# Performance work log

Hardware: AMD Instinct MI355X
Metric: run time of the kernel (lower is better)

## Reference

```python
import jax, jax.numpy as jnp
import numpy as np

D_MODEL = 2048
D_STATE = 16
KER = 4
DT_RANK = D_MODEL // 16  # mamba default: ceil(d_model/16) = 128
B_SZ = 2
SEQ = 1024


def setup_inputs() -> dict:
    key = jax.random.key(0)
    ks = jax.random.split(key, 8)
    s = 0.02
    return {
        "x": jax.random.normal(ks[0], (B_SZ, SEQ, D_MODEL), jnp.float32),
        # in_proj: d_model -> 2*d_inner (expand=1 so d_inner=d_model)
        "W_in": jax.random.normal(ks[1], (2 * D_MODEL, D_MODEL), jnp.float32) * s,
        # depthwise causal conv, one kernel of length KER per channel
        "conv_w": jax.random.normal(ks[2], (D_MODEL, KER), jnp.float32) * s,
        "conv_b": jnp.zeros((D_MODEL,), jnp.float32),
        # x_proj: d_inner -> dt_rank + 2*d_state
        "W_xproj": jax.random.normal(ks[3], (DT_RANK + 2 * D_STATE, D_MODEL), jnp.float32) * s,
        # dt_proj: dt_rank -> d_inner
        "W_dt": jax.random.normal(ks[4], (D_MODEL, DT_RANK), jnp.float32) * s,
        "b_dt": jax.random.uniform(ks[5], (D_MODEL,), jnp.float32, -4.0, -2.0),
        # S4D-real init: A = -[1..d_state] per channel, stored as log
        "A_log": jnp.log(jnp.broadcast_to(jnp.arange(1, D_STATE + 1, dtype=jnp.float32), (D_MODEL, D_STATE))),
        "Dskip": jnp.ones((D_MODEL,), jnp.float32),
        # out_proj: d_inner -> d_model
        "W_out": jax.random.normal(ks[6], (D_MODEL, D_MODEL), jnp.float32) * s,
    }


def _mamba(x, W_in, conv_w, conv_b, W_xproj, W_dt, b_dt, A_log, Dskip, W_out):
    Bsz, L, dm = x.shape
    d_state = A_log.shape[1]
    dt_rank = W_dt.shape[1]
    K = conv_w.shape[1]

    # in_proj -> gate z and ssm input u
    xz = x @ W_in.T                      # [B, L, 2*d_inner]
    u, z = jnp.split(xz, 2, axis=-1)     # each [B, L, d_inner]

    # causal depthwise conv1d over time, then SiLU
    up = jnp.pad(u, ((0, 0), (K - 1, 0), (0, 0)))
    conv = conv_b + sum(conv_w[:, k] * up[:, k:k + L, :] for k in range(K))
    u = jax.nn.silu(conv)                # [B, L, d_inner]

    # input-dependent dt, B, C
    x_dbl = u @ W_xproj.T                # [B, L, dt_rank + 2*d_state]
    dt_r = x_dbl[..., :dt_rank]
    Bm = x_dbl[..., dt_rank:dt_rank + d_state]      # [B, L, N]
    Cm = x_dbl[..., dt_rank + d_state:]             # [B, L, N]
    dt = jax.nn.softplus(dt_r @ W_dt.T + b_dt)      # [B, L, d_inner]

    A = -jnp.exp(A_log)                             # [d_inner, N]
    dA = jnp.exp(dt[..., None] * A)                 # [B, L, d_inner, N]
    dBu = dt[..., None] * Bm[:, :, None, :] * u[..., None]  # [B, L, d_inner, N]

    def step(h, inp):
        dA_t, dBu_t, C_t = inp
        h = dA_t * h + dBu_t                        # [B, d_inner, N]
        y_t = jnp.einsum('bdn,bn->bd', h, C_t)      # [B, d_inner]
        return h, y_t

    h0 = jnp.zeros((Bsz, dm, d_state), dtype=x.dtype)
    _, ys = jax.lax.scan(step, h0,
                         (dA.swapaxes(0, 1), dBu.swapaxes(0, 1), Cm.swapaxes(0, 1)))
    y = ys.swapaxes(0, 1) + u * Dskip               # [B, L, d_inner]
    y = y * jax.nn.silu(z)
    return y @ W_out.T                              # [B, L, d_model]


def reference(x, W_in, conv_w, conv_b, W_xproj, W_dt, b_dt, A_log, Dskip, W_out):
    return _mamba(x, W_in, conv_w, conv_b, W_xproj, W_dt, b_dt, A_log, Dskip, W_out)
```

## Files before the change

### kernel.cpp

```cpp
#include <hip/hip_runtime.h>
#include <hip/hip_bf16.h>


#define D_MODEL 2048
#define D_STATE 16
#define KER 4
#define DT_RANK 128
#define B_SZ 2
#define SEQ 1024
#define BL (B_SZ * SEQ)
#define XPROJ_N (DT_RANK + 2 * D_STATE)
#define NC 32
#define TC (SEQ / NC)

using f32x4  = __attribute__((ext_vector_type(4))) float;
using bf16x8 = __attribute__((ext_vector_type(8))) __bf16;
using bf16x4 = __attribute__((ext_vector_type(4))) __bf16;

__device__ __forceinline__ float softplusf(float x) {
    return (x > 20.f) ? x : log1pf(__expf(x));
}
__device__ __forceinline__ float siluf(float x) {
    return x / (1.f + __expf(-x));
}

__global__ __launch_bounds__(256) void split_kernel(
    const float* __restrict__ src,
    __bf16* __restrict__ hi, __bf16* __restrict__ lo, int n4)
{
    int i = blockIdx.x * 256 + threadIdx.x;
    if (i >= n4) return;
    float4 v = *reinterpret_cast<const float4*>(&src[(size_t)i * 4]);
    bf16x4 hv, lv;
    float f[4] = {v.x, v.y, v.z, v.w};
    #pragma unroll
    for (int j = 0; j < 4; ++j) {
        __bf16 h = (__bf16)f[j];
        hv[j] = h;
        lv[j] = (__bf16)(f[j] - (float)h);
    }
    *reinterpret_cast<bf16x4*>(&hi[(size_t)i * 4]) = hv;
    *reinterpret_cast<bf16x4*>(&lo[(size_t)i * 4]) = lv;
}

__global__ __launch_bounds__(256, 2) void gemm_bf3(
    const __bf16* __restrict__ Ah, const __bf16* __restrict__ Al,
    const __bf16* __restrict__ Wh, const __bf16* __restrict__ Wl,
    float* __restrict__ C, int N_, int K)
{
    __shared__ __align__(16) __bf16 lds[4 * 128 * 64];
    __bf16* sAh = lds;
    __bf16* sAl = lds + 8192;
    __bf16* sWh = lds + 16384;
    __bf16* sWl = lds + 24576;

    const int tid = threadIdx.x;
    const int bm = blockIdx.y * 128;
    const int bn = blockIdx.x * 128;
    const int w  = tid >> 6;
    const int l  = tid & 63;
    const int wr = (w >> 1) * 64;
    const int wc = (w & 1) * 64;
    const int fr = l & 15;
    const int fq = l >> 4;

    f32x4 acc[4][4] = {};

    for (int k0 = 0; k0 < K; k0 += 64) {
        #pragma unroll
        for (int i = 0; i < 4; ++i) {
            const int f  = i * 256 + tid;
            const int r  = f >> 3;
            const int ss = f & 7;
            const int gs = ss ^ (r & 7);
            const size_t ga = (size_t)(bm + r) * K + k0 + gs * 8;
            const size_t gw = (size_t)(bn + r) * K + k0 + gs * 8;
            __builtin_amdgcn_global_load_lds(
                (const __attribute__((address_space(1))) void*)(Ah + ga),
                (__attribute__((address_space(3))) void*)(sAh + (size_t)f * 8), 16, 0, 0);
            __builtin_amdgcn_global_load_lds(
                (const __attribute__((address_space(1))) void*)(Al + ga),
                (__attribute__((address_space(3))) void*)(sAl + (size_t)f * 8), 16, 0, 0);
            __builtin_amdgcn_global_load_lds(
                (const __attribute__((address_space(1))) void*)(Wh + gw),
                (__attribute__((address_space(3))) void*)(sWh + (size_t)f * 8), 16, 0, 0);
            __builtin_amdgcn_global_load_lds(
                (const __attribute__((address_space(1))) void*)(Wl + gw),
                (__attribute__((address_space(3))) void*)(sWl + (size_t)f * 8), 16, 0, 0);
        }
        __syncthreads();

        #pragma unroll
        for (int ks = 0; ks < 2; ++ks) {
            bf16x8 ah[4], al[4], wh[4], wl[4];
            #pragma unroll
            for (int t = 0; t < 4; ++t) {
                const int ra = wr + t * 16 + fr;
                const int sa = (ks * 4 + fq) ^ (ra & 7);
                ah[t] = *reinterpret_cast<const bf16x8*>(&sAh[ra * 64 + sa * 8]);
                al[t] = *reinterpret_cast<const bf16x8*>(&sAl[ra * 64 + sa * 8]);
                const int rw = wc + t * 16 + fr;
                const int sw = (ks * 4 + fq) ^ (rw & 7);
                wh[t] = *reinterpret_cast<const bf16x8*>(&sWh[rw * 64 + sw * 8]);
                wl[t] = *reinterpret_cast<const bf16x8*>(&sWl[rw * 64 + sw * 8]);
            }
            #pragma unroll
            for (int mt = 0; mt < 4; ++mt)
                #pragma unroll
                for (int nt = 0; nt < 4; ++nt) {
                    acc[mt][nt] = __builtin_amdgcn_mfma_f32_16x16x32_bf16(
                        ah[mt], wh[nt], acc[mt][nt], 0, 0, 0);
                    acc[mt][nt] = __builtin_amdgcn_mfma_f32_16x16x32_bf16(
                        ah[mt], wl[nt], acc[mt][nt], 0, 0, 0);
                    acc[mt][nt] = __builtin_amdgcn_mfma_f32_16x16x32_bf16(
                        al[mt], wh[nt], acc[mt][nt], 0, 0, 0);
                }
        }
        __syncthreads();
    }

    #pragma unroll
    for (int mt = 0; mt < 4; ++mt)
        #pragma unroll
        for (int nt = 0; nt < 4; ++nt)
            #pragma unroll
            for (int j = 0; j < 4; ++j)
                C[(size_t)(bm + wr + mt * 16 + fq * 4 + j) * N_
                  + bn + wc + nt * 16 + fr] = acc[mt][nt][j];
}

#define BM 64
#define BN 64
#define BKT 32

template <int EPI>
__global__ __launch_bounds__(256) void gemm_nt(
    const float* __restrict__ A, int lda,
    const float* __restrict__ W, int ldw,
    float* __restrict__ C, int ldc,
    const float* __restrict__ bias,
    int M, int N, int K)
{
    __shared__ float As[BKT][BM + 4];
    __shared__ float Ws[BKT][BN + 4];

    const int tid = threadIdx.x;
    const int bm = blockIdx.y * BM;
    const int bn = blockIdx.x * BN;
    const int tx = tid & 15;
    const int ty = tid >> 4;

    float acc[4][4] = {};

    for (int k0 = 0; k0 < K; k0 += BKT) {
        #pragma unroll
        for (int i = 0; i < 2; ++i) {
            int f = tid + i * 256;
            int row = f >> 3;
            int kq  = f & 7;
            float4 v = *reinterpret_cast<const float4*>(
                &A[(size_t)(bm + row) * lda + k0 + kq * 4]);
            As[kq * 4 + 0][row] = v.x;
            As[kq * 4 + 1][row] = v.y;
            As[kq * 4 + 2][row] = v.z;
            As[kq * 4 + 3][row] = v.w;
        }
        #pragma unroll
        for (int i = 0; i < 2; ++i) {
            int f = tid + i * 256;
            int row = f >> 3;
            int kq  = f & 7;
            int gn = bn + row;
            float4 v = make_float4(0.f, 0.f, 0.f, 0.f);
            if (gn < N) {
                v = *reinterpret_cast<const float4*>(
                    &W[(size_t)gn * ldw + k0 + kq * 4]);
            }
            Ws[kq * 4 + 0][row] = v.x;
            Ws[kq * 4 + 1][row] = v.y;
            Ws[kq * 4 + 2][row] = v.z;
            Ws[kq * 4 + 3][row] = v.w;
        }
        __syncthreads();

        #pragma unroll
        for (int kk = 0; kk < BKT; ++kk) {
            float4 a4 = *reinterpret_cast<const float4*>(&As[kk][ty * 4]);
            float4 w4 = *reinterpret_cast<const float4*>(&Ws[kk][tx * 4]);
            float a[4] = {a4.x, a4.y, a4.z, a4.w};
            float wv[4] = {w4.x, w4.y, w4.z, w4.w};
            #pragma unroll
            for (int i = 0; i < 4; ++i)
                #pragma unroll
                for (int j = 0; j < 4; ++j)
                    acc[i][j] = fmaf(a[i], wv[j], acc[i][j]);
        }
        __syncthreads();
    }

    #pragma unroll
    for (int i = 0; i < 4; ++i) {
        int gm = bm + ty * 4 + i;
        #pragma unroll
        for (int j = 0; j < 4; ++j) {
            int gn = bn + tx * 4 + j;
            if (gn < N) {
                float v = acc[i][j];
                if (EPI == 1) v = softplusf(v + bias[gn]);
                C[(size_t)gm * ldc + gn] = v;
            }
        }
    }
}

#define XBM 64
#define XBN 32
#define XKS 8
#define XKC (D_MODEL / XKS)

__global__ __launch_bounds__(256) void xdbl_partial(
    const float* __restrict__ A,
    const float* __restrict__ W,
    float* __restrict__ P)
{
    __shared__ float As[BKT][XBM + 4];
    __shared__ float Ws[BKT][XBN + 4];

    const int tid = threadIdx.x;
    const int bm = blockIdx.y * XBM;
    const int bn = blockIdx.x * XBN;
    const int ks = blockIdx.z;
    const int tx = tid & 7;
    const int ty = tid >> 3;

    float acc[2][4] = {};

    const int kend = (ks + 1) * XKC;
    for (int k0 = ks * XKC; k0 < kend; k0 += BKT) {
        #pragma unroll
        for (int i = 0; i < 2; ++i) {
            int f = tid + i * 256;
            int row = f >> 3;
            int kq  = f & 7;
            float4 v = *reinterpret_cast<const float4*>(
                &A[(size_t)(bm + row) * D_MODEL + k0 + kq * 4]);
            As[kq * 4 + 0][row] = v.x;
            As[kq * 4 + 1][row] = v.y;
            As[kq * 4 + 2][row] = v.z;
            As[kq * 4 + 3][row] = v.w;
        }
        {
            int row = tid >> 3;
            int kq  = tid & 7;
            float4 v = *reinterpret_cast<const float4*>(
                &W[(size_t)(bn + row) * D_MODEL + k0 + kq * 4]);
            Ws[kq * 4 + 0][row] = v.x;
            Ws[kq * 4 + 1][row] = v.y;
            Ws[kq * 4 + 2][row] = v.z;
            Ws[kq * 4 + 3][row] = v.w;
        }
        __syncthreads();

        #pragma unroll
        for (int kk = 0; kk < BKT; ++kk) {
            float a0 = As[kk][ty * 2 + 0];
            float a1 = As[kk][ty * 2 + 1];
            float4 w4 = *reinterpret_cast<const float4*>(&Ws[kk][tx * 4]);
            float wv[4] = {w4.x, w4.y, w4.z, w4.w};
            #pragma unroll
            for (int j = 0; j < 4; ++j) {
                acc[0][j] = fmaf(a0, wv[j], acc[0][j]);
                acc[1][j] = fmaf(a1, wv[j], acc[1][j]);
            }
        }
        __syncthreads();
    }

    #pragma unroll
    for (int i = 0; i < 2; ++i) {
        const int gm = bm + ty * 2 + i;
        #pragma unroll
        for (int j = 0; j < 4; ++j) {
            const int gn = bn + tx * 4 + j;
            P[((size_t)ks * BL + gm) * XPROJ_N + gn] = acc[i][j];
        }
    }
}

__global__ __launch_bounds__(256) void xdbl_reduce(
    const float* __restrict__ P, float* __restrict__ xdbl)
{
    const int i = blockIdx.x * 256 + threadIdx.x;
    const int n4 = BL * XPROJ_N / 4;
    if (i >= n4) return;
    float4 s = *reinterpret_cast<const float4*>(&P[(size_t)i * 4]);
    #pragma unroll
    for (int ks = 1; ks < XKS; ++ks) {
        float4 v = *reinterpret_cast<const float4*>(
            &P[(size_t)ks * BL * XPROJ_N + (size_t)i * 4]);
        s.x += v.x; s.y += v.y; s.z += v.z; s.w += v.w;
    }
    *reinterpret_cast<float4*>(&xdbl[(size_t)i * 4]) = s;
}

__global__ __launch_bounds__(256) void conv_silu_kernel(
    const float* __restrict__ xz,
    const float* __restrict__ conv_w,
    const float* __restrict__ conv_b,
    float* __restrict__ u)
{
    int idx = blockIdx.x * 256 + threadIdx.x;
    if (idx >= BL * (D_MODEL / 4)) return;
    const int d4 = (idx & (D_MODEL / 4 - 1)) * 4;
    const int bl = idx >> 9;
    const int l  = bl & (SEQ - 1);
    const int b  = bl >> 10;

    float4 cb = *reinterpret_cast<const float4*>(&conv_b[d4]);
    float4 cw[4];
    #pragma unroll
    for (int j = 0; j < 4; ++j)
        cw[j] = *reinterpret_cast<const float4*>(&conv_w[(d4 + j) * KER]);

    float acc[4] = {cb.x, cb.y, cb.z, cb.w};
    #pragma unroll
    for (int k = 0; k < KER; ++k) {
        const int ls = l - (KER - 1) + k;
        if (ls >= 0) {
            float4 v = *reinterpret_cast<const float4*>(
                &xz[(size_t)(b * SEQ + ls) * (2 * D_MODEL) + d4]);
            acc[0] = fmaf((&cw[0].x)[k], v.x, acc[0]);
            acc[1] = fmaf((&cw[1].x)[k], v.y, acc[1]);
            acc[2] = fmaf((&cw[2].x)[k], v.z, acc[2]);
            acc[3] = fmaf((&cw[3].x)[k], v.w, acc[3]);
        }
    }
    float4 o;
    o.x = siluf(acc[0]); o.y = siluf(acc[1]);
    o.z = siluf(acc[2]); o.w = siluf(acc[3]);
    *reinterpret_cast<float4*>(&u[(size_t)bl * D_MODEL + d4]) = o;
}

__global__ __launch_bounds__(256) void scan_part1(
    const float* __restrict__ dt,
    const float* __restrict__ xdbl,
    const float* __restrict__ u,
    const float* __restrict__ A_log,
    float* __restrict__ PH,
    float* __restrict__ Hend)
{
    const int tid = threadIdx.x;
    const int d   = blockIdx.x * 256 + tid;
    const int bc  = blockIdx.y;
    const int b   = bc >> 5;
    const int c   = bc & (NC - 1);

    float A[16];
    #pragma unroll
    for (int q = 0; q < 4; ++q) {
        float4 v = *reinterpret_cast<const float4*>(&A_log[d * 16 + q * 4]);
        A[q*4+0] = -__expf(v.x); A[q*4+1] = -__expf(v.y);
        A[q*4+2] = -__expf(v.z); A[q*4+3] = -__expf(v.w);
    }
    float h[16] = {};
    float P[16];
    #pragma unroll
    for (int n = 0; n < 16; ++n) P[n] = 1.f;

    const size_t row0 = (size_t)b * SEQ + c * TC;
    for (int t = 0; t < TC; ++t) {
        const size_t row = row0 + t;
        const float dtv = dt[row * D_MODEL + d];
        const float uv  = u[row * D_MODEL + d];
        float Bv[16];
        const float4* Bp = reinterpret_cast<const float4*>(&xdbl[row * XPROJ_N + DT_RANK]);
        #pragma unroll
        for (int q = 0; q < 4; ++q) {
            float4 v = Bp[q];
            Bv[q*4+0] = v.x; Bv[q*4+1] = v.y; Bv[q*4+2] = v.z; Bv[q*4+3] = v.w;
        }
        const float dtu = dtv * uv;
        #pragma unroll
        for (int n = 0; n < 16; ++n) {
            float dA = __expf(dtv * A[n]);
            h[n] = fmaf(dA, h[n], dtu * Bv[n]);
            P[n] *= dA;
        }
    }
    const size_t off = ((size_t)bc * D_MODEL + d) * 16;
    #pragma unroll
    for (int q = 0; q < 4; ++q) {
        *reinterpret_cast<float4*>(&PH[off + q*4])   =
            make_float4(P[q*4+0], P[q*4+1], P[q*4+2], P[q*4+3]);
        *reinterpret_cast<float4*>(&Hend[off + q*4]) =
            make_float4(h[q*4+0], h[q*4+1], h[q*4+2], h[q*4+3]);
    }
}

__global__ __launch_bounds__(256) void scan_part2(
    float* __restrict__ PH,
    const float* __restrict__ Hend)
{
    const int g  = blockIdx.x * 256 + threadIdx.x;
    const int b  = g >> 15;
    const int dn = g & 32767;
    float h = 0.f;
    #pragma unroll
    for (int c = 0; c < NC; ++c) {
        const size_t off = ((size_t)(b * NC + c) * D_MODEL * 16) + dn;
        const float p  = PH[off];
        const float he = Hend[off];
        PH[off] = h;
        h = fmaf(p, h, he);
    }
}

__global__ __launch_bounds__(256) void scan_part3(
    const float* __restrict__ dt,
    const float* __restrict__ xdbl,
    const float* __restrict__ xz,
    const float* __restrict__ u,
    const float* __restrict__ A_log,
    const float* __restrict__ Dskip,
    const float* __restrict__ PH,
    __bf16* __restrict__ yh, __bf16* __restrict__ yl)
{
    const int tid = threadIdx.x;
    const int d   = blockIdx.x * 256 + tid;
    const int bc  = blockIdx.y;
    const int b   = bc >> 5;
    const int c   = bc & (NC - 1);

    float A[16];
    #pragma unroll
    for (int q = 0; q < 4; ++q) {
        float4 v = *reinterpret_cast<const float4*>(&A_log[d * 16 + q * 4]);
        A[q*4+0] = -__expf(v.x); A[q*4+1] = -__expf(v.y);
        A[q*4+2] = -__expf(v.z); A[q*4+3] = -__expf(v.w);
    }
    float h[16];
    const size_t off = ((size_t)bc * D_MODEL + d) * 16;
    #pragma unroll
    for (int q = 0; q < 4; ++q) {
        float4 v = *reinterpret_cast<const float4*>(&PH[off + q*4]);
        h[q*4+0] = v.x; h[q*4+1] = v.y; h[q*4+2] = v.z; h[q*4+3] = v.w;
    }
    const float Dk = Dskip[d];

    const size_t row0 = (size_t)b * SEQ + c * TC;
    for (int t = 0; t < TC; ++t) {
        const size_t row = row0 + t;
        const float dtv = dt[row * D_MODEL + d];
        const float uv  = u[row * D_MODEL + d];
        float Bv[16], Cv[16];
        const float4* Bp = reinterpret_cast<const float4*>(&xdbl[row * XPROJ_N + DT_RANK]);
        const float4* Cp = reinterpret_cast<const float4*>(&xdbl[row * XPROJ_N + DT_RANK + D_STATE]);
        #pragma unroll
        for (int q = 0; q < 4; ++q) {
            float4 v = Bp[q];
            Bv[q*4+0] = v.x; Bv[q*4+1] = v.y; Bv[q*4+2] = v.z; Bv[q*4+3] = v.w;
            float4 wv = Cp[q];
            Cv[q*4+0] = wv.x; Cv[q*4+1] = wv.y; Cv[q*4+2] = wv.z; Cv[q*4+3] = wv.w;
        }
        const float dtu = dtv * uv;
        float y = 0.f;
        #pragma unroll
        for (int n = 0; n < 16; ++n) {
            float dA = __expf(dtv * A[n]);
            h[n] = fmaf(dA, h[n], dtu * Bv[n]);
            y = fmaf(h[n], Cv[n], y);
        }
        const float zv = xz[row * (2 * D_MODEL) + D_MODEL + d];
        const float yv = (y + uv * Dk) * siluf(zv);
        const __bf16 hv = (__bf16)yv;
        yh[row * D_MODEL + d] = hv;
        yl[row * D_MODEL + d] = (__bf16)(yv - (float)hv);
    }
}

extern "C" void kernel_launch(void* const* d_in, const int* in_sizes, int n_in,
                              void* d_out, int out_size, void* d_ws, size_t ws_size,
                              hipStream_t stream) {
    const float* x       = (const float*)d_in[0];
    const float* W_in    = (const float*)d_in[1];
    const float* conv_w  = (const float*)d_in[2];
    const float* conv_b  = (const float*)d_in[3];
    const float* W_xproj = (const float*)d_in[4];
    const float* W_dt    = (const float*)d_in[5];
    const float* b_dt    = (const float*)d_in[6];
    const float* A_log   = (const float*)d_in[7];
    const float* Dskip   = (const float*)d_in[8];
    const float* W_out   = (const float*)d_in[9];
    float* out = (float*)d_out;

    float* ws = (float*)d_ws;
    const size_t M1 = 1024 * 1024;
    float* xz   = ws;
    float* u    = ws + 8 * M1;
    float* xdbl = ws + 12 * M1;
    float* dt   = ws + 12 * M1 + 512 * 1024;
    float* PH   = dt + 4 * M1;
    float* Hend = PH + 2 * M1;

    __bf16* planes = (__bf16*)(ws + 25 * M1);
    __bf16* xh  = planes;
    __bf16* xl  = xh + 4 * M1;
    __bf16* wih = xl + 4 * M1;
    __bf16* wil = wih + 8 * M1;
    __bf16* woh = wih;
    __bf16* wol = wih + 4 * M1;
    __bf16* yh  = xh;
    __bf16* yl  = xl;
    float* xpart = (float*)(ws + 25 * M1);

    split_kernel<<<(BL * D_MODEL / 4 + 255) / 256, 256, 0, stream>>>(x, xh, xl, BL * D_MODEL / 4);
    split_kernel<<<(2 * D_MODEL * D_MODEL / 4 + 255) / 256, 256, 0, stream>>>(
        W_in, wih, wil, 2 * D_MODEL * D_MODEL / 4);

    {
        dim3 grid(2 * D_MODEL / 128, BL / 128);
        gemm_bf3<<<grid, 256, 0, stream>>>(xh, xl, wih, wil, xz, 2 * D_MODEL, D_MODEL);
    }
    conv_silu_kernel<<<BL * (D_MODEL / 4) / 256, 256, 0, stream>>>(xz, conv_w, conv_b, u);

    split_kernel<<<(D_MODEL * D_MODEL / 4 + 255) / 256, 256, 0, stream>>>(
        W_out, woh, wol, D_MODEL * D_MODEL / 4);

    {
        dim3 grid(XPROJ_N / XBN, BL / XBM, XKS);
        xdbl_partial<<<grid, 256, 0, stream>>>(u, W_xproj, xpart);
        xdbl_reduce<<<(BL * XPROJ_N / 4 + 255) / 256, 256, 0, stream>>>(xpart, xdbl);
    }
    {
        dim3 grid(D_MODEL / BN, BL / BM);
        gemm_nt<1><<<grid, 256, 0, stream>>>(xdbl, XPROJ_N, W_dt, DT_RANK,
                                             dt, D_MODEL, b_dt,
                                             BL, D_MODEL, DT_RANK);
    }
    {
        dim3 grid(D_MODEL / 256, B_SZ * NC);
        scan_part1<<<grid, 256, 0, stream>>>(dt, xdbl, u, A_log, PH, Hend);
        scan_part2<<<B_SZ * D_MODEL * 16 / 256, 256, 0, stream>>>(PH, Hend);
        scan_part3<<<grid, 256, 0, stream>>>(dt, xdbl, xz, u, A_log, Dskip, PH, yh, yl);
    }
    {
        dim3 grid(D_MODEL / 128, BL / 128);
        gemm_bf3<<<grid, 256, 0, stream>>>(yh, yl, woh, wol, out, D_MODEL, D_MODEL);
    }
}
```

Measured before the change: 403.5 us.

## Use 32x32x16 MFMA in split-bf16 GEMM, remap workgroups, fuse split kernels

The 3-pass split-bf16 GEMM moves from 16x16x32 to 32x32x16 MFMA tiles (2x2 per wave), which changes the LDS fragment loads and the output write mapping. It also adds an XCD-aware remap of workgroup IDs so neighbouring tiles share L2, and merges the x and W_in bf16 split kernels into one grid-stride launch. The aim is fewer LDS reads per MFMA, better cache locality across chiplets and one less launch. The risks are register pressure from 16-wide accumulators and the remap formula assuming the tile count divides evenly by 8.

```diff
diff --git a/kernel.cpp b/kernel.cpp
--- a/kernel.cpp
+++ b/kernel.cpp
@@ -14,6 +14,7 @@
 #define TC (SEQ / NC)
 
 using f32x4  = __attribute__((ext_vector_type(4))) float;
+using f32x16 = __attribute__((ext_vector_type(16))) float;
 using bf16x8 = __attribute__((ext_vector_type(8))) __bf16;
 using bf16x4 = __attribute__((ext_vector_type(4))) __bf16;
 
@@ -24,12 +25,9 @@
     return x / (1.f + __expf(-x));
 }
 
-__global__ __launch_bounds__(256) void split_kernel(
-    const float* __restrict__ src,
-    __bf16* __restrict__ hi, __bf16* __restrict__ lo, int n4)
-{
-    int i = blockIdx.x * 256 + threadIdx.x;
-    if (i >= n4) return;
+__device__ __forceinline__ void split4(const float* __restrict__ src,
+                                       __bf16* __restrict__ hi,
+                                       __bf16* __restrict__ lo, int i) {
     float4 v = *reinterpret_cast<const float4*>(&src[(size_t)i * 4]);
     bf16x4 hv, lv;
     float f[4] = {v.x, v.y, v.z, v.w};
@@ -41,6 +39,28 @@
     }
     *reinterpret_cast<bf16x4*>(&hi[(size_t)i * 4]) = hv;
     *reinterpret_cast<bf16x4*>(&lo[(size_t)i * 4]) = lv;
+}
+
+__global__ __launch_bounds__(256) void split_kernel(
+    const float* __restrict__ src,
+    __bf16* __restrict__ hi, __bf16* __restrict__ lo, int n4)
+{
+    int i = blockIdx.x * 256 + threadIdx.x;
+    if (i >= n4) return;
+    split4(src, hi, lo, i);
+}
+
+__global__ __launch_bounds__(256) void split_xwi_kernel(
+    const float* __restrict__ x,  __bf16* __restrict__ xh,  __bf16* __restrict__ xl,
+    const float* __restrict__ wi, __bf16* __restrict__ wih, __bf16* __restrict__ wil)
+{
+    const int NX = BL * D_MODEL / 4;
+    const int NI = 2 * D_MODEL * D_MODEL / 4;
+    const int total = NX + NI;
+    for (int i = blockIdx.x * 256 + threadIdx.x; i < total; i += gridDim.x * 256) {
+        if (i < NX) split4(x, xh, xl, i);
+        else        split4(wi, wih, wil, i - NX);
+    }
 }
 
 __global__ __launch_bounds__(256, 2) void gemm_bf3(
@@ -55,16 +75,21 @@
     __bf16* sWl = lds + 24576;
 
     const int tid = threadIdx.x;
-    const int bm = blockIdx.y * 128;
-    const int bn = blockIdx.x * 128;
+
+    const int nwg = gridDim.x * gridDim.y;
+    const int fid = blockIdx.y * gridDim.x + blockIdx.x;
+    const int nid = (fid & 7) * (nwg >> 3) + (fid >> 3);
+    const int bm = (nid / gridDim.x) * 128;
+    const int bn = (nid % gridDim.x) * 128;
+
     const int w  = tid >> 6;
     const int l  = tid & 63;
     const int wr = (w >> 1) * 64;
     const int wc = (w & 1) * 64;
-    const int fr = l & 15;
-    const int fq = l >> 4;
-
-    f32x4 acc[4][4] = {};
+    const int lr = l & 31;
+    const int kg = l >> 5;
+
+    f32x16 acc[2][2] = {};
 
     for (int k0 = 0; k0 < K; k0 += 64) {
         #pragma unroll
@@ -91,28 +116,29 @@
         __syncthreads();
 
         #pragma unroll
-        for (int ks = 0; ks < 2; ++ks) {
-            bf16x8 ah[4], al[4], wh[4], wl[4];
+        for (int ks = 0; ks < 4; ++ks) {
+            const int slot = ks * 2 + kg;
+            bf16x8 ah[2], al[2], wh[2], wl[2];
             #pragma unroll
-            for (int t = 0; t < 4; ++t) {
-                const int ra = wr + t * 16 + fr;
-                const int sa = (ks * 4 + fq) ^ (ra & 7);
+            for (int t = 0; t < 2; ++t) {
+                const int ra = wr + t * 32 + lr;
+                const int sa = slot ^ (ra & 7);
                 ah[t] = *reinterpret_cast<const bf16x8*>(&sAh[ra * 64 + sa * 8]);
                 al[t] = *reinterpret_cast<const bf16x8*>(&sAl[ra * 64 + sa * 8]);
-                const int rw = wc + t * 16 + fr;
-                const int sw = (ks * 4 + fq) ^ (rw & 7);
+                const int rw = wc + t * 32 + lr;
+                const int sw = slot ^ (rw & 7);
                 wh[t] = *reinterpret_cast<const bf16x8*>(&sWh[rw * 64 + sw * 8]);
                 wl[t] = *reinterpret_cast<const bf16x8*>(&sWl[rw * 64 + sw * 8]);
             }
             #pragma unroll
-            for (int mt = 0; mt < 4; ++mt)
+            for (int mt = 0; mt < 2; ++mt)
                 #pragma unroll
-                for (int nt = 0; nt < 4; ++nt) {
-                    acc[mt][nt] = __builtin_amdgcn_mfma_f32_16x16x32_bf16(
+                for (int nt = 0; nt < 2; ++nt) {
+                    acc[mt][nt] = __builtin_amdgcn_mfma_f32_32x32x16_bf16(
                         ah[mt], wh[nt], acc[mt][nt], 0, 0, 0);
-                    acc[mt][nt] = __builtin_amdgcn_mfma_f32_16x16x32_bf16(
+                    acc[mt][nt] = __builtin_amdgcn_mfma_f32_32x32x16_bf16(
                         ah[mt], wl[nt], acc[mt][nt], 0, 0, 0);
-                    acc[mt][nt] = __builtin_amdgcn_mfma_f32_16x16x32_bf16(
+                    acc[mt][nt] = __builtin_amdgcn_mfma_f32_32x32x16_bf16(
                         al[mt], wh[nt], acc[mt][nt], 0, 0, 0);
                 }
         }
@@ -120,13 +146,15 @@
     }
 
     #pragma unroll
-    for (int mt = 0; mt < 4; ++mt)
-        #pragma unroll
-        for (int nt = 0; nt < 4; ++nt)
+    for (int mt = 0; mt < 2; ++mt)
+        #pragma unroll
+        for (int nt = 0; nt < 2; ++nt)
             #pragma unroll
-            for (int j = 0; j < 4; ++j)
-                C[(size_t)(bm + wr + mt * 16 + fq * 4 + j) * N_
-                  + bn + wc + nt * 16 + fr] = acc[mt][nt][j];
+            for (int reg = 0; reg < 16; ++reg) {
+                const int row = (reg & 3) + 8 * (reg >> 2) + 4 * kg;
+                C[(size_t)(bm + wr + mt * 32 + row) * N_
+                  + bn + wc + nt * 32 + lr] = acc[mt][nt][reg];
+            }
 }
 
 #define BM 64
@@ -513,9 +541,7 @@
     __bf16* yl  = xl;
     float* xpart = (float*)(ws + 25 * M1);
 
-    split_kernel<<<(BL * D_MODEL / 4 + 255) / 256, 256, 0, stream>>>(x, xh, xl, BL * D_MODEL / 4);
-    split_kernel<<<(2 * D_MODEL * D_MODEL / 4 + 255) / 256, 256, 0, stream>>>(
-        W_in, wih, wil, 2 * D_MODEL * D_MODEL / 4);
+    split_xwi_kernel<<<2048, 256, 0, stream>>>(x, xh, xl, W_in, wih, wil);
 
     {
         dim3 grid(2 * D_MODEL / 128, BL / 128);
```

Result: slower. 424.2 us (+5.1%).
